# Kernel optimization log

Measured on AMD Instinct MI355X. Metric: run time of the kernel, lower is better.

The kernel has to match this reference:

```python
import jax, jax.numpy as jnp
import numpy as np

N_NODES = 100000
N_EDGES = 1600000
D_IN = 128
D_OUT = 128


def setup_inputs() -> dict:
    key = jax.random.key(0)
    k1, k2, k3, k4, k5, k6 = jax.random.split(key, 6)
    stdv = 1.0 / np.sqrt(D_OUT)
    x = jax.random.normal(k1, (N_NODES, D_IN), dtype=jnp.float32)
    weight = jax.random.uniform(k2, (D_IN, D_OUT), minval=-stdv, maxval=stdv, dtype=jnp.float32)
    bias = jax.random.uniform(k3, (D_OUT,), minval=-stdv, maxval=stdv, dtype=jnp.float32)
    edge_vals = jax.random.uniform(k4, (N_EDGES,), dtype=jnp.float32)
    edge_rows = jax.random.randint(k5, (N_EDGES,), 0, N_NODES, dtype=jnp.int32)
    edge_cols = jax.random.randint(k6, (N_EDGES,), 0, N_NODES, dtype=jnp.int32)
    return {"x": x, "weight": weight, "bias": bias,
            "edge_vals": edge_vals, "edge_rows": edge_rows, "edge_cols": edge_cols}


def reference(x, weight, bias, edge_vals, edge_rows, edge_cols):
    # Dense projection: support = X W  -> [N, D_OUT]
    support = jnp.matmul(x, weight)
    # Sparse adjacency matmul (COO SpMM): out[r] += A[r,c] * support[c]
    gathered = edge_vals[:, None] * support[edge_cols]  # [E, D_OUT]
    out = jax.ops.segment_sum(gathered, edge_rows, num_segments=N_NODES)
    return out + bias
```

## Files before the change

kernel.cpp:

```cpp
#include <hip/hip_runtime.h>
#include <hip/hip_bf16.h>

#define N_NODES 100000
#define N_EDGES 1600000
#define D 128
#define NBUCK 782
#define G 320
#define EPB 5000
#define CAPG 16
#define WSLOT (G * CAPG)
#define EBCAP 2816
#define OCAP 8192

typedef short  s8v  __attribute__((ext_vector_type(8)));
typedef float  f4v  __attribute__((ext_vector_type(4)));

__device__ __forceinline__ ushort f2bf(float f) {
    uint u = __float_as_uint(f);
    return (ushort)((u + 0x7FFFu + ((u >> 16) & 1u)) >> 16);
}
__device__ __forceinline__ float bflo(uint u) { return __uint_as_float(u << 16); }
__device__ __forceinline__ float bfhi(uint u) { return __uint_as_float(u & 0xFFFF0000u); }

__global__ __launch_bounds__(256) void k_wt(const float* __restrict__ w,
                                            ushort* __restrict__ wt,
                                            int* __restrict__ ocur) {
    int i = blockIdx.x * 256 + threadIdx.x;
    if (i == 0) *ocur = 0;
    if (i < D * D) {
        int k = i >> 7, n = i & 127;
        wt[n * D + k] = f2bf(w[i]);
    }
}

__global__ __launch_bounds__(256, 4) void k_gemm(const float* __restrict__ x,
                                                 const ushort* __restrict__ wt,
                                                 ushort* __restrict__ supb) {
    __shared__ int4 Bl4[2048];
    char* Bl = (char*)Bl4;

    const int t    = threadIdx.x;
    const int lane = t & 63;
    const int w    = t >> 6;
    const int row0 = blockIdx.x * 128;

    const int4* g = (const int4*)wt;
    #pragma unroll
    for (int i = 0; i < 8; ++i) {
        int idx = t + i * 256;
        int n = idx >> 4, c = idx & 15;
        *(int4*)(Bl + ((n * 256 + c * 16) ^ ((n & 7) << 4))) = g[idx];
    }
    __syncthreads();

    f4v acc[2][8] = {};
    const int arow = row0 + w * 32 + (lane & 15);
    const int kb   = (lane >> 4) * 8;

    #pragma unroll
    for (int ks = 0; ks < 4; ++ks) {
        s8v a[2];
        #pragma unroll
        for (int m = 0; m < 2; ++m) {
            int r = arow + m * 16;
            float4 f0 = make_float4(0.f, 0.f, 0.f, 0.f);
            float4 f1 = make_float4(0.f, 0.f, 0.f, 0.f);
            if (r < N_NODES) {
                const float4* p = (const float4*)(x + (size_t)r * D + ks * 32 + kb);
                f0 = p[0];
                f1 = p[1];
            }
            s8v av;
            av[0] = (short)f2bf(f0.x); av[1] = (short)f2bf(f0.y);
            av[2] = (short)f2bf(f0.z); av[3] = (short)f2bf(f0.w);
            av[4] = (short)f2bf(f1.x); av[5] = (short)f2bf(f1.y);
            av[6] = (short)f2bf(f1.z); av[7] = (short)f2bf(f1.w);
            a[m] = av;
        }
        #pragma unroll
        for (int n = 0; n < 8; ++n) {
            int brow = n * 16 + (lane & 15);
            s8v b = *(s8v*)(Bl + ((brow * 256 + (ks * 32 + kb) * 2) ^ ((brow & 7) << 4)));
            acc[0][n] = __builtin_amdgcn_mfma_f32_16x16x32_bf16(a[0], b, acc[0][n], 0, 0, 0);
            acc[1][n] = __builtin_amdgcn_mfma_f32_16x16x32_bf16(a[1], b, acc[1][n], 0, 0, 0);
        }
    }

    __syncthreads();
    char* E = Bl + w * 8192;
    #pragma unroll
    for (int m = 0; m < 2; ++m)
        #pragma unroll
        for (int n = 0; n < 8; ++n)
            #pragma unroll
            for (int r = 0; r < 4; ++r) {
                int rl  = m * 16 + ((lane >> 4) << 2) + r;
                int col = n * 16 + (lane & 15);
                *(ushort*)(E + ((rl * 256 + col * 2) ^ ((rl & 7) << 4))) =
                    f2bf(acc[m][n][r]);
            }
    __syncthreads();
    #pragma unroll
    for (int i = 0; i < 8; ++i) {
        int idx = lane + i * 64;
        int rl = idx >> 4, c = idx & 15;
        int4 v = *(int4*)(E + ((rl * 256 + c * 16) ^ ((rl & 7) << 4)));
        int grow = row0 + w * 32 + rl;
        if (grow < N_NODES)
            *(int4*)((char*)supb + (size_t)grow * 256 + c * 16) = v;
    }
}

__global__ __launch_bounds__(512) void k_part(const int* __restrict__ er,
                                              const int* __restrict__ ec,
                                              const float* __restrict__ ev,
                                              int2* __restrict__ tmp,
                                              int* __restrict__ counts,
                                              int* __restrict__ ocur,
                                              int4* __restrict__ ovf) {
    __shared__ int cur[NBUCK];
    const int tx = (int)threadIdx.x;
    const int g  = blockIdx.x;
    for (int i = tx; i < NBUCK; i += 512) cur[i] = 0;
    __syncthreads();

    const int base = g * EPB;
    for (int i = tx; i < EPB; i += 512) {
        int e = base + i;
        int   r = er[e];
        int   c = ec[e];
        float v = ev[e];
        int b = r >> 7;
        int p = atomicAdd(&cur[b], 1);
        if (p < CAPG) {
            tmp[(size_t)b * WSLOT + g * CAPG + p] =
                make_int2(((r & 127) << 17) | c, __float_as_int(v));
        } else {
            int o = atomicAdd(ocur, 1);
            if (o < OCAP) ovf[o] = make_int4(r, c, __float_as_int(v), 0);
        }
    }
    __syncthreads();
    for (int i = tx; i < NBUCK; i += 512) {
        int n = cur[i];
        counts[g * NBUCK + i] = (n > CAPG) ? CAPG : n;
    }
}

__global__ __launch_bounds__(320) void k_sort(int2* __restrict__ tmp,
                                              const int* __restrict__ counts,
                                              int2* __restrict__ rowrg,
                                              int* __restrict__ ocur,
                                              int4* __restrict__ ovf) {
    __shared__ int wn[G];
    __shared__ int wincl[G];
    __shared__ int hist[128], ex[128], cur[128];
    __shared__ int2 eb[EBCAP];
    const int tx = (int)threadIdx.x;
    const int b  = blockIdx.x;
    const int r0 = b << 7;

    int n = counts[tx * NBUCK + b];
    wn[tx] = n;
    wincl[tx] = n;
    if (tx < 128) { hist[tx] = 0; cur[tx] = 0; }
    __syncthreads();

    for (int off = 1; off < G; off <<= 1) {
        int t = (tx >= off) ? wincl[tx - off] : 0;
        __syncthreads();
        wincl[tx] += t;
        __syncthreads();
    }
    const int cnt0 = wincl[G - 1];

    {
        int o = wincl[tx] - wn[tx];
        const int2* win = tmp + ((size_t)b * G + tx) * CAPG;
        for (int k = 0; k < wn[tx]; ++k) {
            int idx = o + k;
            int2 t = win[k];
            if (idx < EBCAP) {
                eb[idx] = t;
            } else {
                int oo = atomicAdd(ocur, 1);
                if (oo < OCAP)
                    ovf[oo] = make_int4(r0 + (t.x >> 17), t.x & 0x1FFFF, t.y, 0);
            }
        }
    }
    __syncthreads();
    const int cnt = (cnt0 > EBCAP) ? EBCAP : cnt0;

    for (int i = tx; i < cnt; i += 320)
        atomicAdd(&hist[eb[i].x >> 17], 1);
    __syncthreads();

    int hv = (tx < 128) ? hist[tx] : 0;
    if (tx < 128) ex[tx] = hv;
    __syncthreads();
    for (int off = 1; off < 128; off <<= 1) {
        int t = 0;
        if (tx < 128 && tx >= off) t = ex[tx - off];
        __syncthreads();
        if (tx < 128) ex[tx] += t;
        __syncthreads();
    }
    if (tx < 128) {
        int incl = ex[tx];
        int e0   = incl - hv;
        if (r0 + tx < N_NODES)
            rowrg[r0 + tx] = make_int2(b * WSLOT + e0, b * WSLOT + incl);
        ex[tx] = e0;
    }
    __syncthreads();

    int2* dst = tmp + (size_t)b * WSLOT;
    for (int i = tx; i < cnt; i += 320) {
        int2 t = eb[i];
        int lr = t.x >> 17;
        int p  = ex[lr] + atomicAdd(&cur[lr], 1);
        dst[p] = make_int2(t.x & 0x1FFFF, t.y);
    }
}

__global__ __launch_bounds__(256) void k_spmm(const ushort* __restrict__ supb,
                                              const int2* __restrict__ rowrg,
                                              const int2* __restrict__ scv,
                                              const float* __restrict__ bias,
                                              float* __restrict__ out) {
    const int row = blockIdx.x * 4 + (threadIdx.x >> 6);
    if (row >= N_NODES) return;
    const int lane = threadIdx.x & 63;
    const int sub  = lane >> 5;
    const int sl   = lane & 31;

    const int2 rg = rowrg[row];
    int j = rg.x;
    const int end = rg.y;
    const uint2* S = (const uint2*)supb;

    float4 acc = make_float4(0.f, 0.f, 0.f, 0.f);

    for (; j + 7 < end; j += 8) {
        int2 e0 = scv[j + sub];
        int2 e1 = scv[j + 2 + sub];
        int2 e2 = scv[j + 4 + sub];
        int2 e3 = scv[j + 6 + sub];
        uint2 s0 = S[(size_t)e0.x * 32 + sl];
        uint2 s1 = S[(size_t)e1.x * 32 + sl];
        uint2 s2 = S[(size_t)e2.x * 32 + sl];
        uint2 s3 = S[(size_t)e3.x * 32 + sl];
        float v0 = __int_as_float(e0.y), v1 = __int_as_float(e1.y);
        float v2 = __int_as_float(e2.y), v3 = __int_as_float(e3.y);
        acc.x += v0 * bflo(s0.x) + v1 * bflo(s1.x) + v2 * bflo(s2.x) + v3 * bflo(s3.x);
        acc.y += v0 * bfhi(s0.x) + v1 * bfhi(s1.x) + v2 * bfhi(s2.x) + v3 * bfhi(s3.x);
        acc.z += v0 * bflo(s0.y) + v1 * bflo(s1.y) + v2 * bflo(s2.y) + v3 * bflo(s3.y);
        acc.w += v0 * bfhi(s0.y) + v1 * bfhi(s1.y) + v2 * bfhi(s2.y) + v3 * bfhi(s3.y);
    }
    for (; j < end; j += 2) {
        int jj = j + sub;
        if (jj > end - 1) jj = end - 1;
        int2 e = scv[jj];
        float v = (j + sub < end) ? __int_as_float(e.y) : 0.f;
        uint2 s = S[(size_t)e.x * 32 + sl];
        acc.x += v * bflo(s.x);
        acc.y += v * bfhi(s.x);
        acc.z += v * bflo(s.y);
        acc.w += v * bfhi(s.y);
    }

    acc.x += __shfl_xor(acc.x, 32);
    acc.y += __shfl_xor(acc.y, 32);
    acc.z += __shfl_xor(acc.z, 32);
    acc.w += __shfl_xor(acc.w, 32);

    if (sub == 0) {
        float4 bb = *(const float4*)(bias + 4 * sl);
        acc.x += bb.x; acc.y += bb.y; acc.z += bb.z; acc.w += bb.w;
        *(float4*)(out + (size_t)row * D + 4 * sl) = acc;
    }
}

__global__ __launch_bounds__(256) void k_ofl(const ushort* __restrict__ supb,
                                             const int4* __restrict__ ovf,
                                             const int* __restrict__ ocur,
                                             float* __restrict__ out) {
    int n = *ocur;
    if (n > OCAP) n = OCAP;
    const int lane = threadIdx.x & 63;
    const uint* S = (const uint*)supb;
    for (int e = (blockIdx.x * 256 + threadIdx.x) >> 6; e < n; e += 64) {
        int4 rec = ovf[e];
        uint s = S[(size_t)rec.y * 64 + lane];
        float v = __int_as_float(rec.z);
        atomicAdd(&out[(size_t)rec.x * D + 2 * lane],     v * bflo(s));
        atomicAdd(&out[(size_t)rec.x * D + 2 * lane + 1], v * bfhi(s));
    }
}

extern "C" void kernel_launch(void* const* d_in, const int* in_sizes, int n_in,
                              void* d_out, int out_size, void* d_ws, size_t ws_size,
                              hipStream_t stream) {
    const float* x    = (const float*)d_in[0];
    const float* w    = (const float*)d_in[1];
    const float* bias = (const float*)d_in[2];
    const float* ev   = (const float*)d_in[3];
    const int*   er   = (const int*)d_in[4];
    const int*   ec   = (const int*)d_in[5];
    float* out = (float*)d_out;

    char* ws = (char*)d_ws;
    ushort* supb   = (ushort*)(ws);
    ushort* wt     = (ushort*)(ws + 25600000);
    int*    counts = (int*)   (ws + 25632768);
    int*    ocur   = (int*)   (ws + 26633728);
    int4*   ovf    = (int4*)  (ws + 26633792);
    int2*   tmp    = (int2*)  (ws + 26764864);
    int2*   rowrg  = (int2*)  (ws + 58795584);

    k_wt  <<<64, 256, 0, stream>>>(w, wt, ocur);
    k_gemm<<<(N_NODES + 127) / 128, 256, 0, stream>>>(x, wt, supb);

    k_part<<<G, 512, 0, stream>>>(er, ec, ev, tmp, counts, ocur, ovf);
    k_sort<<<NBUCK, 320, 0, stream>>>(tmp, counts, rowrg, ocur, ovf);

    k_spmm<<<(N_NODES + 3) / 4, 256, 0, stream>>>(supb, rowrg, tmp, bias, out);
    k_ofl <<<16, 256, 0, stream>>>(supb, ovf, ocur, out);
}
```

Baseline: 140.5 us.

## Fuse dense GEMM and edge partition kernels into one heterogeneous launch

The GEMM and COO edge-partition kernels become a single launch. The first NBUCK blocks compute the bf16 X·W projection and the remaining G blocks bucket edges by row block. The two independent stages can then run concurrently on the GPU, and one kernel launch and its serialization gap go away. In exchange the partition blocks drop from 512 to 256 threads, and shared memory is a 32KB union sized for the GEMM, which may reduce occupancy for the partition work.

New measurement: 135.8 us. 1.03x faster.

```diff
diff --git a/kernel.cpp b/kernel.cpp
--- a/kernel.cpp
+++ b/kernel.cpp
@@ -33,117 +33,118 @@
     }
 }
 
-__global__ __launch_bounds__(256, 4) void k_gemm(const float* __restrict__ x,
+__global__ __launch_bounds__(256, 4) void k_fuse(const float* __restrict__ x,
                                                  const ushort* __restrict__ wt,
-                                                 ushort* __restrict__ supb) {
-    __shared__ int4 Bl4[2048];
-    char* Bl = (char*)Bl4;
-
-    const int t    = threadIdx.x;
-    const int lane = t & 63;
-    const int w    = t >> 6;
-    const int row0 = blockIdx.x * 128;
-
-    const int4* g = (const int4*)wt;
-    #pragma unroll
-    for (int i = 0; i < 8; ++i) {
-        int idx = t + i * 256;
-        int n = idx >> 4, c = idx & 15;
-        *(int4*)(Bl + ((n * 256 + c * 16) ^ ((n & 7) << 4))) = g[idx];
-    }
-    __syncthreads();
-
-    f4v acc[2][8] = {};
-    const int arow = row0 + w * 32 + (lane & 15);
-    const int kb   = (lane >> 4) * 8;
-
-    #pragma unroll
-    for (int ks = 0; ks < 4; ++ks) {
-        s8v a[2];
+                                                 ushort* __restrict__ supb,
+                                                 const int* __restrict__ er,
+                                                 const int* __restrict__ ec,
+                                                 const float* __restrict__ ev,
+                                                 int2* __restrict__ tmp,
+                                                 int* __restrict__ counts,
+                                                 int* __restrict__ ocur,
+                                                 int4* __restrict__ ovf) {
+    __shared__ __attribute__((aligned(16))) char smem[32768];
+
+    const int t = (int)threadIdx.x;
+
+    if (blockIdx.x < NBUCK) {
+        char* Bl = smem;
+        const int lane = t & 63;
+        const int w    = t >> 6;
+        const int row0 = blockIdx.x * 128;
+
+        const int4* g4 = (const int4*)wt;
         #pragma unroll
-        for (int m = 0; m < 2; ++m) {
-            int r = arow + m * 16;
-            float4 f0 = make_float4(0.f, 0.f, 0.f, 0.f);
-            float4 f1 = make_float4(0.f, 0.f, 0.f, 0.f);
-            if (r < N_NODES) {
-                const float4* p = (const float4*)(x + (size_t)r * D + ks * 32 + kb);
-                f0 = p[0];
-                f1 = p[1];
+        for (int i = 0; i < 8; ++i) {
+            int idx = t + i * 256;
+            int n = idx >> 4, c = idx & 15;
+            *(int4*)(Bl + ((n * 256 + c * 16) ^ ((n & 7) << 4))) = g4[idx];
+        }
+        __syncthreads();
+
+        f4v acc[2][8] = {};
+        const int arow = row0 + w * 32 + (lane & 15);
+        const int kb   = (lane >> 4) * 8;
+
+        #pragma unroll
+        for (int ks = 0; ks < 4; ++ks) {
+            s8v a[2];
+            #pragma unroll
+            for (int m = 0; m < 2; ++m) {
+                int r = arow + m * 16;
+                float4 f0 = make_float4(0.f, 0.f, 0.f, 0.f);
+                float4 f1 = make_float4(0.f, 0.f, 0.f, 0.f);
+                if (r < N_NODES) {
+                    const float4* p = (const float4*)(x + (size_t)r * D + ks * 32 + kb);
+                    f0 = p[0];
+                    f1 = p[1];
+                }
+                s8v av;
+                av[0] = (short)f2bf(f0.x); av[1] = (short)f2bf(f0.y);
+                av[2] = (short)f2bf(f0.z); av[3] = (short)f2bf(f0.w);
+                av[4] = (short)f2bf(f1.x); av[5] = (short)f2bf(f1.y);
+                av[6] = (short)f2bf(f1.z); av[7] = (short)f2bf(f1.w);
+                a[m] = av;
             }
-            s8v av;
-            av[0] = (short)f2bf(f0.x); av[1] = (short)f2bf(f0.y);
-            av[2] = (short)f2bf(f0.z); av[3] = (short)f2bf(f0.w);
-            av[4] = (short)f2bf(f1.x); av[5] = (short)f2bf(f1.y);
-            av[6] = (short)f2bf(f1.z); av[7] = (short)f2bf(f1.w);
-            a[m] = av;
-        }
+            #pragma unroll
+            for (int n = 0; n < 8; ++n) {
+                int brow = n * 16 + (lane & 15);
+                s8v b = *(s8v*)(Bl + ((brow * 256 + (ks * 32 + kb) * 2) ^ ((brow & 7) << 4)));
+                acc[0][n] = __builtin_amdgcn_mfma_f32_16x16x32_bf16(a[0], b, acc[0][n], 0, 0, 0);
+                acc[1][n] = __builtin_amdgcn_mfma_f32_16x16x32_bf16(a[1], b, acc[1][n], 0, 0, 0);
+            }
+        }
+
+        __syncthreads();
+        char* E = Bl + w * 8192;
         #pragma unroll
-        for (int n = 0; n < 8; ++n) {
-            int brow = n * 16 + (lane & 15);
-            s8v b = *(s8v*)(Bl + ((brow * 256 + (ks * 32 + kb) * 2) ^ ((brow & 7) << 4)));
-            acc[0][n] = __builtin_amdgcn_mfma_f32_16x16x32_bf16(a[0], b, acc[0][n], 0, 0, 0);
-            acc[1][n] = __builtin_amdgcn_mfma_f32_16x16x32_bf16(a[1], b, acc[1][n], 0, 0, 0);
-        }
-    }
-
-    __syncthreads();
-    char* E = Bl + w * 8192;
-    #pragma unroll
-    for (int m = 0; m < 2; ++m)
+        for (int m = 0; m < 2; ++m)
+            #pragma unroll
+            for (int n = 0; n < 8; ++n)
+                #pragma unroll
+                for (int r = 0; r < 4; ++r) {
+                    int rl  = m * 16 + ((lane >> 4) << 2) + r;
+                    int col = n * 16 + (lane & 15);
+                    *(ushort*)(E + ((rl * 256 + col * 2) ^ ((rl & 7) << 4))) =
+                        f2bf(acc[m][n][r]);
+                }
+        __syncthreads();
         #pragma unroll
-        for (int n = 0; n < 8; ++n)
-            #pragma unroll
-            for (int r = 0; r < 4; ++r) {
-                int rl  = m * 16 + ((lane >> 4) << 2) + r;
-                int col = n * 16 + (lane & 15);
-                *(ushort*)(E + ((rl * 256 + col * 2) ^ ((rl & 7) << 4))) =
-                    f2bf(acc[m][n][r]);
+        for (int i = 0; i < 8; ++i) {
+            int idx = lane + i * 64;
+            int rl = idx >> 4, c = idx & 15;
+            int4 v = *(int4*)(E + ((rl * 256 + c * 16) ^ ((rl & 7) << 4)));
+            int grow = row0 + w * 32 + rl;
+            if (grow < N_NODES)
+                *(int4*)((char*)supb + (size_t)grow * 256 + c * 16) = v;
+        }
+    } else {
+        int* cur = (int*)smem;
+        const int g = blockIdx.x - NBUCK;
+        for (int i = t; i < NBUCK; i += 256) cur[i] = 0;
+        __syncthreads();
+
+        const int base = g * EPB;
+        for (int i = t; i < EPB; i += 256) {
+            int e = base + i;
+            int   r = er[e];
+            int   c = ec[e];
+            float v = ev[e];
+            int b = r >> 7;
+            int p = atomicAdd(&cur[b], 1);
+            if (p < CAPG) {
+                tmp[(size_t)b * WSLOT + g * CAPG + p] =
+                    make_int2(((r & 127) << 17) | c, __float_as_int(v));
+            } else {
+                int o = atomicAdd(ocur, 1);
+                if (o < OCAP) ovf[o] = make_int4(r, c, __float_as_int(v), 0);
             }
-    __syncthreads();
-    #pragma unroll
-    for (int i = 0; i < 8; ++i) {
-        int idx = lane + i * 64;
-        int rl = idx >> 4, c = idx & 15;
-        int4 v = *(int4*)(E + ((rl * 256 + c * 16) ^ ((rl & 7) << 4)));
-        int grow = row0 + w * 32 + rl;
-        if (grow < N_NODES)
-            *(int4*)((char*)supb + (size_t)grow * 256 + c * 16) = v;
-    }
-}
-
-__global__ __launch_bounds__(512) void k_part(const int* __restrict__ er,
-                                              const int* __restrict__ ec,
-                                              const float* __restrict__ ev,
-                                              int2* __restrict__ tmp,
-                                              int* __restrict__ counts,
-                                              int* __restrict__ ocur,
-                                              int4* __restrict__ ovf) {
-    __shared__ int cur[NBUCK];
-    const int tx = (int)threadIdx.x;
-    const int g  = blockIdx.x;
-    for (int i = tx; i < NBUCK; i += 512) cur[i] = 0;
-    __syncthreads();
-
-    const int base = g * EPB;
-    for (int i = tx; i < EPB; i += 512) {
-        int e = base + i;
-        int   r = er[e];
-        int   c = ec[e];
-        float v = ev[e];
-        int b = r >> 7;
-        int p = atomicAdd(&cur[b], 1);
-        if (p < CAPG) {
-            tmp[(size_t)b * WSLOT + g * CAPG + p] =
-                make_int2(((r & 127) << 17) | c, __float_as_int(v));
-        } else {
-            int o = atomicAdd(ocur, 1);
-            if (o < OCAP) ovf[o] = make_int4(r, c, __float_as_int(v), 0);
-        }
-    }
-    __syncthreads();
-    for (int i = tx; i < NBUCK; i += 512) {
-        int n = cur[i];
-        counts[g * NBUCK + i] = (n > CAPG) ? CAPG : n;
+        }
+        __syncthreads();
+        for (int i = t; i < NBUCK; i += 256) {
+            int n = cur[i];
+            counts[g * NBUCK + i] = (n > CAPG) ? CAPG : n;
+        }
     }
 }
 
@@ -320,9 +321,8 @@
     int2*   rowrg  = (int2*)  (ws + 58795584);
 
     k_wt  <<<64, 256, 0, stream>>>(w, wt, ocur);
-    k_gemm<<<(N_NODES + 127) / 128, 256, 0, stream>>>(x, wt, supb);
-
-    k_part<<<G, 512, 0, stream>>>(er, ec, ev, tmp, counts, ocur, ovf);
+    k_fuse<<<NBUCK + G, 256, 0, stream>>>(x, wt, supb, er, ec, ev, tmp,
+                                          counts, ocur, ovf);
     k_sort<<<NBUCK, 320, 0, stream>>>(tmp, counts, rowrg, ocur, ovf);
 
     k_spmm<<<(N_NODES + 3) / 4, 256, 0, stream>>>(supb, rowrg, tmp, bias, out);
```
